# Performance work log

Hardware: AMD Instinct MI355X
Metric: run time of the kernel (lower is better)

Reference implementation:

```python
import jax, jax.numpy as jnp
import numpy as np

N_HEADS = 8
DIM_HEAD = 64


def _lin_params(key, fan_in, fan_out):
    k1, k2 = jax.random.split(key)
    w = jax.random.normal(k1, (fan_out, fan_in), jnp.float32) * 0.02
    b = jax.random.normal(k2, (fan_out,), jnp.float32) * 0.02
    return w, b


def setup_inputs() -> dict:
    key = jax.random.key(0)
    ks = jax.random.split(key, 16)
    n_nodes, n_edges = 30000, 480000
    input_nf, output_nf, hidden_nf = 128, 128, 256
    hd = N_HEADS * DIM_HEAD
    inp = {}
    inp['h'] = jax.random.normal(ks[0], (n_nodes, input_nf), jnp.float32)
    inp['x'] = jax.random.normal(ks[1], (n_nodes, 3), jnp.float32)
    inp['edge_index'] = jax.random.randint(ks[2], (2, n_edges), 0, n_nodes, jnp.int64)
    inp['mask'] = jnp.ones((n_edges,), jnp.bool_)
    inp['wq'], inp['bq'] = _lin_params(ks[3], input_nf, hd)
    inp['wk'], inp['bk'] = _lin_params(ks[4], input_nf, hd)
    inp['wv'], inp['bv'] = _lin_params(ks[5], input_nf, hd)
    inp['wo'], inp['bo'] = _lin_params(ks[6], hd, output_nf)
    inp['pw1'], inp['pb1'] = _lin_params(ks[7], 6, hidden_nf)
    inp['pw2'], inp['pb2'] = _lin_params(ks[8], hidden_nf, N_HEADS)
    inp['ew1'], inp['eb1'] = _lin_params(ks[9], 2 * input_nf + 7, hidden_nf)
    inp['ew2'], inp['eb2'] = _lin_params(ks[10], hidden_nf, hidden_nf)
    inp['eww'], inp['ewb'] = _lin_params(ks[11], hidden_nf, N_HEADS)
    inp['cw1'], inp['cb1'] = _lin_params(ks[12], 3, hidden_nf)
    inp['cw2'], inp['cb2'] = _lin_params(ks[13], hidden_nf, hidden_nf)
    inp['cw3'], inp['cb3'] = _lin_params(ks[14], hidden_nf, output_nf)
    return inp


def reference(h, x, edge_index, mask,
              wq, bq, wk, bk, wv, bv, wo, bo,
              pw1, pb1, pw2, pb2,
              ew1, eb1, ew2, eb2, eww, ewb,
              cw1, cb1, cw2, cb2, cw3, cb3):
    n_nodes = h.shape[0]
    row, col = edge_index[0], edge_index[1]
    # node projections -> [n, H, D]
    q = (h @ wq.T + bq).reshape(n_nodes, N_HEADS, DIM_HEAD)
    k = (h @ wk.T + bk).reshape(n_nodes, N_HEADS, DIM_HEAD)
    v = (h @ wv.T + bv).reshape(n_nodes, N_HEADS, DIM_HEAD)
    xr, xc = x[row], x[col]
    # pos encoding [E, H]
    abs_pos = jnp.concatenate([xr, xc], axis=-1)
    pos_enc = jax.nn.silu(abs_pos @ pw1.T + pb1) @ pw2.T + pb2
    # edge features -> per-head edge weights [E, H]
    rel_dist = jnp.sum((xr - xc) ** 2, axis=-1, keepdims=True)
    edge_attr = jnp.concatenate([h[row], h[col], rel_dist, xr, xc], axis=-1)
    edge_feat = jax.nn.silu(edge_attr @ ew1.T + eb1) @ ew2.T + eb2
    edge_w = edge_feat @ eww.T + ewb
    # attention scores [E, H]
    score = jnp.einsum('ehd,ehd->eh', q[row], k[col]) / (DIM_HEAD ** 0.5)
    score = score + pos_enc + edge_w
    score = jnp.where(mask[:, None], score, jnp.float32(-1e9))
    # scatter-softmax over edges grouped by destination (row)
    smax = jax.ops.segment_max(score, row, num_segments=n_nodes)
    escore = jnp.exp(score - smax[row])
    ssum = jax.ops.segment_sum(escore, row, num_segments=n_nodes)
    attn = escore / (ssum[row] + 1e-8)
    # weighted aggregation [n, H, D]
    agg = jax.ops.segment_sum(attn[:, :, None] * v[col], row, num_segments=n_nodes)
    out = agg.reshape(n_nodes, -1) @ wo.T + bo
    coord = jax.nn.silu(x @ cw1.T + cb1)
    coord = jax.nn.silu(coord @ cw2.T + cb2)
    coord = coord @ cw3.T + cb3
    return out + coord, jnp.zeros_like(x)
```

## Files before the change

### kernel.cpp

```cpp
#include <hip/hip_runtime.h>

typedef unsigned int uint;
typedef unsigned short ushort;
typedef unsigned char uchar;
typedef __attribute__((ext_vector_type(8))) short bf16x8;
typedef __attribute__((ext_vector_type(8))) ushort ushort8;
typedef __attribute__((ext_vector_type(4))) float f32x4;

__device__ __forceinline__ float silu_fast(float t) {
  return t * __builtin_amdgcn_rcpf(1.f + __expf(-t));
}
__device__ __forceinline__ float bf2f(ushort u) {
  union { uint i; float f; } v; v.i = ((uint)u) << 16; return v.f;
}
__device__ __forceinline__ ushort f2bf(float f) {
  union { float f; uint i; } v; v.f = f;
  uint r = (v.i + 0x7fffu + ((v.i >> 16) & 1u)) >> 16;
  return (ushort)r;
}
__device__ __forceinline__ uchar f2e4m3(float f) {
  uint u = __float_as_uint(f);
  uint s = (u >> 24) & 0x80u;
  uint m = u & 0x7fffffffu;
  if (m >= 0x43f00000u) return (uchar)(s | 0x7e);
  if (m >= 0x3c800000u) {
    uint r = m + 0x7ffffu + ((m >> 20) & 1u);
    uint e = (r >> 23) - 120u;
    if (e > 15u) return (uchar)(s | 0x7e);
    return (uchar)(s | (e << 3) | ((r >> 20) & 7u));
  }
  float az = __uint_as_float(m);
  uint k = (uint)__float2int_rn(az * 512.f);
  return (uchar)(s | k);
}
__device__ __forceinline__ float e4m3f(uint b) {
  uint u = ((b & 0x80u) << 24) | ((b & 0x7fu) << 20);
  return __uint_as_float(u) * 0x1p+120f;
}

__global__ __launch_bounds__(256) void mega_prep(
    const float* __restrict__ h, const float* __restrict__ x,
    const int* __restrict__ ei,
    const float* __restrict__ wq, const float* __restrict__ wk, const float* __restrict__ wv,
    const float* __restrict__ bq, const float* __restrict__ bk, const float* __restrict__ bv,
    const float* __restrict__ ew1, const float* __restrict__ eb1,
    const float* __restrict__ pw1, const float* __restrict__ pb1,
    const float* __restrict__ ew2, const float* __restrict__ eww,
    const float* __restrict__ eb2, const float* __restrict__ ewb,
    const float* __restrict__ pw2, const float* __restrict__ pb2,
    const float* __restrict__ wo, const float* __restrict__ cw3,
    const float* __restrict__ bo, const float* __restrict__ cb3,
    const float* __restrict__ cw1, const float* __restrict__ cb1,
    const float* __restrict__ cw2,
    ushort* __restrict__ h_bf, ushort* __restrict__ c1,
    ushort* __restrict__ wqkv, float* __restrict__ bqkv,
    short* __restrict__ W1T, float* __restrict__ b1big,
    short* __restrict__ W2T, float* __restrict__ biasC,
    ushort* __restrict__ wcomb, float* __restrict__ bcomb,
    ushort* __restrict__ cw2bf, int* __restrict__ cnt,
    int n, int E,
    int o1, int o2, int o3, int o4, int o5, int o6, int o7)
{
  int b = blockIdx.x, tid = threadIdx.x;
  if (b < o1) {
    int idx = b * 256 + tid;
    if (idx * 4 < n * 128) {
      float4 v = *(const float4*)(h + idx * 4);
      ushort4 o; o.x = f2bf(v.x); o.y = f2bf(v.y); o.z = f2bf(v.z); o.w = f2bf(v.w);
      *(ushort4*)(h_bf + idx * 4) = o;
    }
  } else if (b < o2) {
    int idx = (b - o1) * 256 + tid;
    if (idx < n * 256) {
      int node = idx >> 8, j = idx & 255;
      float t = fmaf(x[node * 3 + 2], cw1[j * 3 + 2],
                fmaf(x[node * 3 + 1], cw1[j * 3 + 1],
                fmaf(x[node * 3 + 0], cw1[j * 3 + 0], cb1[j])));
      c1[idx] = f2bf(silu_fast(t));
    }
  } else if (b < o3) {
    int idx = (b - o2) * 256 + tid;
    if (idx < 1536 * 128) {
      int j = idx >> 7, k = idx & 127;
      float v = (j < 512) ? wq[j * 128 + k]
              : (j < 1024) ? wk[(j - 512) * 128 + k]
              : wv[(j - 1024) * 128 + k];
      wqkv[idx] = f2bf(v);
      if (idx < 1536)
        bqkv[idx] = (idx < 512) ? bq[idx] : (idx < 1024) ? bk[idx - 512] : bv[idx - 1024];
    }
  } else if (b < o4) {
    int idx = (b - o3) * 256 + tid;
    if (idx < 512 * 288) {
      int nn = idx / 288, k = idx % 288;
      float v = 0.f;
      if (nn < 256) { if (k < 263) v = ew1[nn * 263 + k]; }
      else          { if (k >= 257 && k < 263) v = pw1[(nn - 256) * 6 + (k - 257)]; }
      W1T[idx] = (short)f2bf(v);
      if (idx < 512) b1big[idx] = (idx < 256) ? eb1[idx] : pb1[idx - 256];
    }
  } else if (b < o5) {
    int idx = (b - o4) * 256 + tid;
    if (idx < 16 * 512) {
      int hh = idx >> 9, k = idx & 511;
      float v = 0.f;
      if (hh < 8) {
        if (k < 256) {
          float s = 0.f;
          for (int j = 0; j < 256; ++j) s += eww[hh * 256 + j] * ew2[j * 256 + k];
          v = s;
        } else v = pw2[hh * 256 + (k - 256)];
      }
      W2T[idx] = (short)f2bf(v);
      if (idx < 16) {
        float bb = 0.f;
        if (idx < 8) {
          float s = 0.f;
          for (int j = 0; j < 256; ++j) s += eww[idx * 256 + j] * eb2[j];
          bb = s + ewb[idx] + pb2[idx];
        }
        biasC[idx] = bb;
      }
    }
  } else if (b < o6) {
    int idx = (b - o5) * 256 + tid;
    if (idx < 128 * 768) {
      int j = idx / 768, k = idx % 768;
      float v = (k < 512) ? wo[j * 512 + k] : cw3[j * 256 + (k - 512)];
      wcomb[idx] = f2bf(v);
      if (idx < 128) bcomb[idx] = bo[idx] + cb3[idx];
    }
  } else if (b < o7) {
    int idx = (b - o6) * 256 + tid;
    if (idx < 256 * 256) cw2bf[idx] = f2bf(cw2[idx]);
  } else {
    int e = (b - o7) * 256 + tid;
    if (e < E) atomicAdd(&cnt[ei[e]], 1);
  }
}

__global__ __launch_bounds__(256) void qkv_mfma2_kernel(
    const ushort* __restrict__ h_bf,
    const ushort* __restrict__ wqkv,
    const float* __restrict__ bqkv,
    ushort* __restrict__ q_t, uchar* __restrict__ k8, ushort* __restrict__ v_t,
    int n)
{
  int tid = threadIdx.x;
  int lane = tid & 63, w = tid >> 6;
  int l15 = lane & 15, l4 = lane >> 4;
  int m0 = blockIdx.x * 64;
  int mrow = m0 + w * 16 + l15;
  bool valid = mrow < n;
  int mr = valid ? mrow : (n - 1);

  bf16x8 hf[4];
#pragma unroll
  for (int ks = 0; ks < 4; ++ks)
    hf[ks] = *(const bf16x8*)(h_bf + (size_t)mr * 128 + ks * 32 + l4 * 8);

  for (int jb = 0; jb < 24; ++jb) {
    f32x4 acc[4];
#pragma unroll
    for (int nf = 0; nf < 4; ++nf) acc[nf] = (f32x4){0.f, 0.f, 0.f, 0.f};
#pragma unroll
    for (int nf = 0; nf < 4; ++nf)
#pragma unroll
      for (int ks = 0; ks < 4; ++ks) {
        bf16x8 wf = *(const bf16x8*)(wqkv + (size_t)(jb * 64 + nf * 16 + l15) * 128 + ks * 32 + l4 * 8);
        acc[nf] = __builtin_amdgcn_mfma_f32_16x16x32_bf16(wf, hf[ks], acc[nf], 0, 0, 0);
      }
    if (valid) {
#pragma unroll
      for (int nf = 0; nf < 4; ++nf) {
        int gc = jb * 64 + nf * 16 + l4 * 4;
        float4 bb = *(const float4*)(bqkv + gc);
        float v0 = acc[nf][0] + bb.x, v1 = acc[nf][1] + bb.y;
        float v2 = acc[nf][2] + bb.z, v3 = acc[nf][3] + bb.w;
        if (jb < 8) {
          ushort4 st; st.x = f2bf(v0); st.y = f2bf(v1); st.z = f2bf(v2); st.w = f2bf(v3);
          *(ushort4*)(q_t + (size_t)mrow * 512 + gc) = st;
        } else if (jb < 16) {
          uint pk = (uint)f2e4m3(v0) | ((uint)f2e4m3(v1) << 8)
                  | ((uint)f2e4m3(v2) << 16) | ((uint)f2e4m3(v3) << 24);
          *(uint*)(k8 + (size_t)mrow * 512 + (gc - 512)) = pk;
        } else {
          ushort4 st; st.x = f2bf(v0); st.y = f2bf(v1); st.z = f2bf(v2); st.w = f2bf(v3);
          *(ushort4*)(v_t + (size_t)mrow * 512 + (gc - 1024)) = st;
        }
      }
    }
  }
}

#define EB 64
#define GS 32
#define TS 72

__global__ __launch_bounds__(256, 4) void edge_mfma2_kernel(
    const ushort* __restrict__ h_bf, const float* __restrict__ x,
    const int* __restrict__ ei, int E,
    const short* __restrict__ W1T, const float* __restrict__ b1big,
    const short* __restrict__ W2T, const float* __restrict__ biasC,
    float* __restrict__ scores)
{
  __shared__ short geomL[EB * GS];
  __shared__ short T1[4 * EB * TS];
  float* slab = (float*)T1;

  int tid = threadIdx.x;
  int lane = tid & 63, w = tid >> 6;
  int l15 = lane & 15, l4 = lane >> 4;
  int eb0 = blockIdx.x * EB;

  if (tid < EB) {
    int eg = min(eb0 + tid, E - 1);
    int r = ei[eg], c = ei[E + eg];
    float xr0 = x[r*3], xr1 = x[r*3+1], xr2 = x[r*3+2];
    float xc0 = x[c*3], xc1 = x[c*3+1], xc2 = x[c*3+2];
    float d0 = xr0-xc0, d1 = xr1-xc1, d2 = xr2-xc2;
    bf16x8 g;
    g[0] = (short)f2bf(d0*d0 + d1*d1 + d2*d2);
    g[1] = (short)f2bf(xr0); g[2] = (short)f2bf(xr1); g[3] = (short)f2bf(xr2);
    g[4] = (short)f2bf(xc0); g[5] = (short)f2bf(xc1); g[6] = (short)f2bf(xc2);
    g[7] = 0;
    bf16x8 z = {0,0,0,0,0,0,0,0};
    *(bf16x8*)(geomL + tid * GS) = g;
    *(bf16x8*)(geomL + tid * GS + 8) = z;
    *(bf16x8*)(geomL + tid * GS + 16) = z;
    *(bf16x8*)(geomL + tid * GS + 24) = z;
  }
  __syncthreads();

  const char* hb = (const char*)h_bf;
  uint ro[4], co[4], ga[4];
#pragma unroll
  for (int ef = 0; ef < 4; ++ef) {
    int eg = min(eb0 + ef * 16 + l15, E - 1);
    int r = ei[eg], c = ei[E + eg];
    ro[ef] = (uint)r * 256 + l4 * 16;
    co[ef] = (uint)c * 256 + l4 * 16;
    ga[ef] = (uint)(ef * 16 + l15) * (GS * 2) + l4 * 16;
  }

  f32x4 sacc[4];
#pragma unroll
  for (int ef = 0; ef < 4; ++ef) sacc[ef] = (f32x4){0.f, 0.f, 0.f, 0.f};

  short* t1w = T1 + w * (EB * TS);

#pragma unroll
  for (int cch = 0; cch < 2; ++cch) {
    const int n0 = cch ? (256 + w * 64) : (w * 64);
    const int ks0 = cch ? 8 : 0;
    f32x4 acc[4][4];
#pragma unroll
    for (int mf = 0; mf < 4; ++mf)
#pragma unroll
      for (int ef = 0; ef < 4; ++ef) acc[mf][ef] = (f32x4){0.f, 0.f, 0.f, 0.f};

#pragma unroll
    for (int ks = ks0; ks < 9; ++ks) {
      bf16x8 aW[4], bE[4];
#pragma unroll
      for (int mf = 0; mf < 4; ++mf)
        aW[mf] = *(const bf16x8*)(W1T + (size_t)(n0 + mf * 16 + l15) * 288 + ks * 32 + l4 * 8);
#pragma unroll
      for (int ef = 0; ef < 4; ++ef) {
        if (ks < 4)      bE[ef] = *(const bf16x8*)(hb + ro[ef] + ks * 64);
        else if (ks < 8) bE[ef] = *(const bf16x8*)(hb + co[ef] + (ks - 4) * 64);
        else             bE[ef] = *(const bf16x8*)((const char*)geomL + ga[ef]);
      }
#pragma unroll
      for (int mf = 0; mf < 4; ++mf)
#pragma unroll
        for (int ef = 0; ef < 4; ++ef)
          acc[mf][ef] = __builtin_amdgcn_mfma_f32_16x16x32_bf16(aW[mf], bE[ef], acc[mf][ef], 0, 0, 0);
    }
#pragma unroll
    for (int mf = 0; mf < 4; ++mf) {
      int nl = mf * 16 + l4 * 4;
      float4 bias = *(const float4*)(b1big + n0 + nl);
#pragma unroll
      for (int ef = 0; ef < 4; ++ef) {
        int e = ef * 16 + l15;
        f32x4 v = acc[mf][ef];
        float s0 = silu_fast(v[0] + bias.x);
        float s1 = silu_fast(v[1] + bias.y);
        float s2 = silu_fast(v[2] + bias.z);
        float s3 = silu_fast(v[3] + bias.w);
        uint2 pk;
        asm("v_cvt_pk_bf16_f32 %0, %1, %2" : "=v"(pk.x) : "v"(s0), "v"(s1));
        asm("v_cvt_pk_bf16_f32 %0, %1, %2" : "=v"(pk.y) : "v"(s2), "v"(s3));
        *(uint2*)(t1w + e * TS + nl) = pk;
      }
    }
#pragma unroll
    for (int ks2 = 0; ks2 < 2; ++ks2) {
      bf16x8 bW2 = *(const bf16x8*)(W2T + (size_t)l15 * 512 + n0 + ks2 * 32 + l4 * 8);
#pragma unroll
      for (int ef = 0; ef < 4; ++ef) {
        bf16x8 aT = *(const bf16x8*)(t1w + (ef * 16 + l15) * TS + ks2 * 32 + l4 * 8);
        sacc[ef] = __builtin_amdgcn_mfma_f32_16x16x32_bf16(aT, bW2, sacc[ef], 0, 0, 0);
      }
    }
  }
  __syncthreads();
#pragma unroll
  for (int ef = 0; ef < 4; ++ef)
#pragma unroll
    for (int i = 0; i < 4; ++i)
      slab[(w * EB + ef * 16 + l4 * 4 + i) * 16 + l15] = sacc[ef][i];
  __syncthreads();
  for (int t = tid; t < EB * 8; t += 256) {
    int e = t >> 3, hh = t & 7;
    float s = biasC[hh]
            + slab[(0 * EB + e) * 16 + hh] + slab[(1 * EB + e) * 16 + hh]
            + slab[(2 * EB + e) * 16 + hh] + slab[(3 * EB + e) * 16 + hh];
    if (eb0 + e < E) scores[(size_t)(eb0 + e) * 8 + hh] = s;
  }
}

__global__ __launch_bounds__(1024) void scan_kernel(int* __restrict__ cnt,
                                                    int* __restrict__ offs, int n) {
  __shared__ int part[1024];
  int t = threadIdx.x;
  int chunk = (n + 1023) >> 10;
  int s = t * chunk, e = min(s + chunk, n);
  int sum = 0;
  for (int i = s; i < e; ++i) sum += cnt[i];
  part[t] = sum;
  __syncthreads();
  for (int off = 1; off < 1024; off <<= 1) {
    int v = (t >= off) ? part[t - off] : 0;
    __syncthreads();
    part[t] += v;
    __syncthreads();
  }
  int run = (t == 0) ? 0 : part[t - 1];
  for (int i = s; i < e; ++i) {
    int c = cnt[i];
    offs[i] = run;
    cnt[i] = run;
    run += c;
  }
  if (t == 1023) offs[n] = run;
}

__global__ __launch_bounds__(256) void fill_kernel(const int* __restrict__ ei,
                                                   int* __restrict__ cursor,
                                                   int2* __restrict__ pairs, int E) {
  int e = blockIdx.x * 256 + threadIdx.x;
  if (e < E) {
    int p = atomicAdd(&cursor[ei[e]], 1);
    pairs[p] = make_int2(e, ei[E + e]);
  }
}

__global__ __launch_bounds__(256) void attn_fused_kernel(
    const int* __restrict__ offs,
    const int2* __restrict__ pairs,
    const int* __restrict__ mask,
    const float* __restrict__ scores,
    const ushort* __restrict__ q_t,
    const uchar* __restrict__ k8,
    const ushort* __restrict__ v_t,
    ushort* __restrict__ agg, int n)
{
  int node = blockIdx.x * 4 + (threadIdx.x >> 6);
  if (node >= n) return;
  int lane = threadIdx.x & 63;
  int start = offs[node], end = offs[node + 1];

  bf16x8 qv = *(const bf16x8*)(q_t + (size_t)node * 512 + lane * 8);
  float qf[8];
#pragma unroll
  for (int j = 0; j < 8; ++j) qf[j] = bf2f((ushort)qv[j]);

  float m = -3.0e38f, ssum = 0.f;
  float acc[8];
#pragma unroll
  for (int j = 0; j < 8; ++j) acc[j] = 0.f;

  if (start < end) {
    int2 pr = pairs[start];
    uint2 kw = *(const uint2*)(k8 + (size_t)pr.y * 512 + lane * 8);
    bf16x8 vv = *(const bf16x8*)(v_t + (size_t)pr.y * 512 + lane * 8);
    float sml = scores[(size_t)pr.x * 8 + (lane >> 3)];
    int mk = mask[pr.x];

    for (int i = start; i < end; ++i) {
      uint2 kwc = kw; bf16x8 vvc = vv; float smlc = sml; int mkc = mk;
      int inx = (i + 1 < end) ? (i + 1) : i;
      pr = pairs[inx];
      kw = *(const uint2*)(k8 + (size_t)pr.y * 512 + lane * 8);
      vv = *(const bf16x8*)(v_t + (size_t)pr.y * 512 + lane * 8);
      sml = scores[(size_t)pr.x * 8 + (lane >> 3)];
      mk = mask[pr.x];

      float dot = 0.f;
#pragma unroll
      for (int j = 0; j < 4; ++j)
        dot = fmaf(qf[j], e4m3f((kwc.x >> (8 * j)) & 0xffu), dot);
#pragma unroll
      for (int j = 0; j < 4; ++j)
        dot = fmaf(qf[4 + j], e4m3f((kwc.y >> (8 * j)) & 0xffu), dot);
      dot += __shfl_xor(dot, 1);
      dot += __shfl_xor(dot, 2);
      dot += __shfl_xor(dot, 4);
      float s = mkc ? fmaf(dot, 0.125f, smlc) : -1e9f;
      float nm = fmaxf(m, s);
      float cs = __expf(m - nm);
      float e  = __expf(s - nm);
      ssum = fmaf(ssum, cs, e);
#pragma unroll
      for (int j = 0; j < 8; ++j)
        acc[j] = fmaf(acc[j], cs, e * bf2f((ushort)vvc[j]));
      m = nm;
    }
  }
  float inv = __builtin_amdgcn_rcpf(ssum + 1e-8f);
  ushort8 ov;
#pragma unroll
  for (int j = 0; j < 8; ++j) ov[j] = f2bf(acc[j] * inv);
  *(ushort8*)(agg + (size_t)node * 512 + lane * 8) = ov;
}

__global__ __launch_bounds__(256) void c2_mfma_kernel(const ushort* __restrict__ c1,
                                                      const ushort* __restrict__ cw2bf,
                                                      const float* __restrict__ cb2,
                                                      ushort* __restrict__ c2, int n) {
  __shared__ float oS[64 * 68];
  int tid = threadIdx.x;
  int lane = tid & 63, w = tid >> 6;
  int l15 = lane & 15, l4 = lane >> 4;
  int m0 = blockIdx.x * 64;
  int n0 = blockIdx.y * 64 + w * 16;

  f32x4 acc[4];
#pragma unroll
  for (int mf = 0; mf < 4; ++mf) acc[mf] = (f32x4){0.f, 0.f, 0.f, 0.f};
#pragma unroll
  for (int ks = 0; ks < 8; ++ks) {
    bf16x8 bW = *(const bf16x8*)(cw2bf + (size_t)(n0 + l15) * 256 + ks * 32 + l4 * 8);
#pragma unroll
    for (int mf = 0; mf < 4; ++mf) {
      int gr = m0 + mf * 16 + l15; if (gr >= n) gr = n - 1;
      bf16x8 aH = *(const bf16x8*)(c1 + (size_t)gr * 256 + ks * 32 + l4 * 8);
      acc[mf] = __builtin_amdgcn_mfma_f32_16x16x32_bf16(aH, bW, acc[mf], 0, 0, 0);
    }
  }
#pragma unroll
  for (int mf = 0; mf < 4; ++mf)
#pragma unroll
    for (int i = 0; i < 4; ++i)
      oS[(mf * 16 + l4 * 4 + i) * 68 + w * 16 + l15] = acc[mf][i];
  __syncthreads();
  {
    int row = tid >> 2, cs = (tid & 3) * 16;
    int gr = m0 + row;
    if (gr < n) {
      int gc = blockIdx.y * 64 + cs;
      ushort8 o0, o1;
#pragma unroll
      for (int j = 0; j < 8; ++j) o0[j] = f2bf(silu_fast(oS[row * 68 + cs + j] + cb2[gc + j]));
#pragma unroll
      for (int j = 0; j < 8; ++j) o1[j] = f2bf(silu_fast(oS[row * 68 + cs + 8 + j] + cb2[gc + 8 + j]));
      *(ushort8*)(c2 + (size_t)gr * 256 + gc) = o0;
      *(ushort8*)(c2 + (size_t)gr * 256 + gc + 8) = o1;
    }
  }
}

__global__ __launch_bounds__(256) void final_mfma_kernel(const ushort* __restrict__ agg,
                                                         const ushort* __restrict__ c2,
                                                         const ushort* __restrict__ wcomb,
                                                         const float* __restrict__ bcomb,
                                                         float* __restrict__ out, int n) {
  __shared__ float oS[64 * 68];
  int tid = threadIdx.x;
  int lane = tid & 63, w = tid >> 6;
  int l15 = lane & 15, l4 = lane >> 4;
  int m0 = blockIdx.x * 64;
  int jb = blockIdx.y;
  int n0 = jb * 64 + w * 16;

  f32x4 acc[4];
#pragma unroll
  for (int mf = 0; mf < 4; ++mf) acc[mf] = (f32x4){0.f, 0.f, 0.f, 0.f};
#pragma unroll
  for (int ks = 0; ks < 24; ++ks) {
    bf16x8 bW = *(const bf16x8*)(wcomb + (size_t)(n0 + l15) * 768 + ks * 32 + l4 * 8);
#pragma unroll
    for (int mf = 0; mf < 4; ++mf) {
      int gr = m0 + mf * 16 + l15; if (gr >= n) gr = n - 1;
      const ushort* ap = (ks < 16) ? (agg + (size_t)gr * 512 + ks * 32)
                                   : (c2 + (size_t)gr * 256 + (ks - 16) * 32);
      bf16x8 aH = *(const bf16x8*)(ap + l4 * 8);
      acc[mf] = __builtin_amdgcn_mfma_f32_16x16x32_bf16(aH, bW, acc[mf], 0, 0, 0);
    }
  }
#pragma unroll
  for (int mf = 0; mf < 4; ++mf)
#pragma unroll
    for (int i = 0; i < 4; ++i)
      oS[(mf * 16 + l4 * 4 + i) * 68 + w * 16 + l15] = acc[mf][i];
  __syncthreads();
  {
    int row = tid >> 2, cs = (tid & 3) * 16;
    int gr = m0 + row;
    if (gr < n) {
      int gc = jb * 64 + cs;
#pragma unroll
      for (int g = 0; g < 4; ++g) {
        float4 o;
        o.x = oS[row * 68 + cs + g * 4 + 0] + bcomb[gc + g * 4 + 0];
        o.y = oS[row * 68 + cs + g * 4 + 1] + bcomb[gc + g * 4 + 1];
        o.z = oS[row * 68 + cs + g * 4 + 2] + bcomb[gc + g * 4 + 2];
        o.w = oS[row * 68 + cs + g * 4 + 3] + bcomb[gc + g * 4 + 3];
        *(float4*)(out + (size_t)gr * 128 + gc + g * 4) = o;
      }
    }
  }
}

extern "C" void kernel_launch(void* const* d_in, const int* in_sizes, int n_in,
                              void* d_out, int out_size, void* d_ws, size_t ws_size,
                              hipStream_t stream) {
  const float* h   = (const float*)d_in[0];
  const float* x   = (const float*)d_in[1];
  const int*   ei  = (const int*)d_in[2];
  const int*   mask= (const int*)d_in[3];
  const float* wq  = (const float*)d_in[4];
  const float* bq  = (const float*)d_in[5];
  const float* wk  = (const float*)d_in[6];
  const float* bk  = (const float*)d_in[7];
  const float* wv  = (const float*)d_in[8];
  const float* bv  = (const float*)d_in[9];
  const float* wo  = (const float*)d_in[10];
  const float* bo  = (const float*)d_in[11];
  const float* pw1 = (const float*)d_in[12];
  const float* pb1 = (const float*)d_in[13];
  const float* pw2 = (const float*)d_in[14];
  const float* pb2 = (const float*)d_in[15];
  const float* ew1 = (const float*)d_in[16];
  const float* eb1 = (const float*)d_in[17];
  const float* ew2 = (const float*)d_in[18];
  const float* eb2 = (const float*)d_in[19];
  const float* eww = (const float*)d_in[20];
  const float* ewb = (const float*)d_in[21];
  const float* cw1 = (const float*)d_in[22];
  const float* cb1 = (const float*)d_in[23];
  const float* cw2 = (const float*)d_in[24];
  const float* cb2 = (const float*)d_in[25];
  const float* cw3 = (const float*)d_in[26];
  const float* cb3 = (const float*)d_in[27];

  int n = in_sizes[0] / 128;
  int E = in_sizes[3];

  char* wptr = (char*)d_ws;
  auto alloc = [&](size_t bytes) {
    char* p = wptr;
    wptr += (bytes + 255) & ~(size_t)255;
    return p;
  };
  ushort* q_t   = (ushort*)alloc((size_t)n * 512 * 2);
  uchar*  k8    = (uchar*)alloc((size_t)n * 512);
  ushort* v_t   = (ushort*)alloc((size_t)n * 512 * 2);
  ushort* h_bf  = (ushort*)alloc((size_t)n * 128 * 2);
  float* scores = (float*)alloc((size_t)E * 8 * 4);
  ushort* agg   = (ushort*)alloc((size_t)n * 512 * 2);
  ushort* c1    = (ushort*)alloc((size_t)n * 256 * 2);
  ushort* c2    = (ushort*)alloc((size_t)n * 256 * 2);
  ushort* wqkv  = (ushort*)alloc((size_t)1536 * 128 * 2);
  float* bqkv   = (float*)alloc((size_t)1536 * 4);
  short* W1T    = (short*)alloc((size_t)512 * 288 * 2);
  float* b1big  = (float*)alloc((size_t)512 * 4);
  short* W2T    = (short*)alloc((size_t)16 * 512 * 2);
  float* biasC  = (float*)alloc((size_t)16 * 4);
  ushort* wcomb = (ushort*)alloc((size_t)128 * 768 * 2);
  float* bcomb  = (float*)alloc((size_t)128 * 4);
  ushort* cw2bf = (ushort*)alloc((size_t)256 * 256 * 2);
  int* offs     = (int*)alloc((size_t)(n + 1) * 4);
  int* cursor   = (int*)alloc((size_t)n * 4);
  int2* pairs   = (int2*)alloc((size_t)E * 8);

  hipMemsetAsync(cursor, 0, (size_t)n * 4, stream);

  int b_h2  = (n * 128 / 4 + 255) / 256;
  int b_c1  = (n * 256 + 255) / 256;
  int b_wq  = (1536 * 128 + 255) / 256;
  int b_w1  = (512 * 288 + 255) / 256;
  int b_w2  = (16 * 512 + 255) / 256;
  int b_wc  = (128 * 768 + 255) / 256;
  int b_cw  = (256 * 256 + 255) / 256;
  int b_cnt = (E + 255) / 256;
  int o1 = b_h2, o2 = o1 + b_c1, o3 = o2 + b_wq, o4 = o3 + b_w1;
  int o5 = o4 + b_w2, o6 = o5 + b_wc, o7 = o6 + b_cw;
  int total_blocks = o7 + b_cnt;

  mega_prep<<<dim3(total_blocks), 256, 0, stream>>>(
      h, x, ei, wq, wk, wv, bq, bk, bv, ew1, eb1, pw1, pb1, ew2, eww, eb2, ewb,
      pw2, pb2, wo, cw3, bo, cb3, cw1, cb1, cw2,
      h_bf, c1, wqkv, bqkv, W1T, b1big, W2T, biasC, wcomb, bcomb, cw2bf, cursor,
      n, E, o1, o2, o3, o4, o5, o6, o7);

  scan_kernel<<<dim3(1), 1024, 0, stream>>>(cursor, offs, n);
  fill_kernel<<<dim3((E + 255) / 256), 256, 0, stream>>>(ei, cursor, pairs, E);

  qkv_mfma2_kernel<<<dim3((n + 63) / 64), 256, 0, stream>>>(h_bf, wqkv, bqkv, q_t, k8, v_t, n);

  edge_mfma2_kernel<<<dim3((E + EB - 1) / EB), 256, 0, stream>>>(
      h_bf, x, ei, E, W1T, b1big, W2T, biasC, scores);

  attn_fused_kernel<<<dim3((n + 3) / 4), 256, 0, stream>>>(
      offs, pairs, mask, scores, q_t, k8, v_t, agg, n);

  c2_mfma_kernel<<<dim3((n + 63) / 64, 4), 256, 0, stream>>>(c1, cw2bf, cb2, c2, n);

  hipMemsetAsync((float*)d_out + (size_t)n * 128, 0, (size_t)n * 3 * 4, stream);
  final_mfma_kernel<<<dim3((n + 63) / 64, 2), 256, 0, stream>>>(agg, c2, wcomb, bcomb,
                                                                (float*)d_out, n);
}
```

Before: 701.0 us.

## Factor edge MLP first layer into per-node projections gathered per edge

The first edge-MLP layer applied to [h[row], h[col]] is split algebraically into two node-level projections (P1 = h·W_row, P2 = h·W_col). These are computed in the node projection GEMM alongside Q/K/V, so each edge only gathers two 256-wide bf16 rows instead of doing a K=256 GEMM. The edge kernel now walks edges in CSR (sorted) order, folds the mask into the pairs array, and writes scores contiguously so attention reads them sequentially. The separate h-to-bf16 conversion pass goes away, and agg reuses the q_t buffer. In exchange it adds bf16 rounding of the partial sums and extra node-level storage.

```diff
diff --git a/kernel.cpp b/kernel.cpp
--- a/kernel.cpp
+++ b/kernel.cpp
@@ -13,10 +13,19 @@
 __device__ __forceinline__ float bf2f(ushort u) {
   union { uint i; float f; } v; v.i = ((uint)u) << 16; return v.f;
 }
+__device__ __forceinline__ float bf2f_lo(uint u) {
+  union { uint i; float f; } v; v.i = u << 16; return v.f;
+}
+__device__ __forceinline__ float bf2f_hi(uint u) {
+  union { uint i; float f; } v; v.i = u & 0xffff0000u; return v.f;
+}
 __device__ __forceinline__ ushort f2bf(float f) {
   union { float f; uint i; } v; v.f = f;
   uint r = (v.i + 0x7fffu + ((v.i >> 16) & 1u)) >> 16;
   return (ushort)r;
+}
+__device__ __forceinline__ uint cvtpk_bf(float a, float b) {
+  uint r; asm("v_cvt_pk_bf16_f32 %0, %1, %2" : "=v"(r) : "v"(a), "v"(b)); return r;
 }
 __device__ __forceinline__ uchar f2e4m3(float f) {
   uint u = __float_as_uint(f);
@@ -39,8 +48,7 @@
 }
 
 __global__ __launch_bounds__(256) void mega_prep(
-    const float* __restrict__ h, const float* __restrict__ x,
-    const int* __restrict__ ei,
+    const float* __restrict__ x, const int* __restrict__ ei,
     const float* __restrict__ wq, const float* __restrict__ wk, const float* __restrict__ wv,
     const float* __restrict__ bq, const float* __restrict__ bk, const float* __restrict__ bv,
     const float* __restrict__ ew1, const float* __restrict__ eb1,
@@ -52,25 +60,18 @@
     const float* __restrict__ bo, const float* __restrict__ cb3,
     const float* __restrict__ cw1, const float* __restrict__ cb1,
     const float* __restrict__ cw2,
-    ushort* __restrict__ h_bf, ushort* __restrict__ c1,
-    ushort* __restrict__ wqkv, float* __restrict__ bqkv,
-    short* __restrict__ W1T, float* __restrict__ b1big,
+    ushort* __restrict__ c1,
+    ushort* __restrict__ wnode, float* __restrict__ bqkv,
+    short* __restrict__ W1g,
     short* __restrict__ W2T, float* __restrict__ biasC,
     ushort* __restrict__ wcomb, float* __restrict__ bcomb,
     ushort* __restrict__ cw2bf, int* __restrict__ cnt,
     int n, int E,
-    int o1, int o2, int o3, int o4, int o5, int o6, int o7)
+    int o1, int o2, int o3, int o4, int o5, int o6)
 {
   int b = blockIdx.x, tid = threadIdx.x;
   if (b < o1) {
     int idx = b * 256 + tid;
-    if (idx * 4 < n * 128) {
-      float4 v = *(const float4*)(h + idx * 4);
-      ushort4 o; o.x = f2bf(v.x); o.y = f2bf(v.y); o.z = f2bf(v.z); o.w = f2bf(v.w);
-      *(ushort4*)(h_bf + idx * 4) = o;
-    }
-  } else if (b < o2) {
-    int idx = (b - o1) * 256 + tid;
     if (idx < n * 256) {
       int node = idx >> 8, j = idx & 255;
       float t = fmaf(x[node * 3 + 2], cw1[j * 3 + 2],
@@ -78,29 +79,37 @@
                 fmaf(x[node * 3 + 0], cw1[j * 3 + 0], cb1[j])));
       c1[idx] = f2bf(silu_fast(t));
     }
+  } else if (b < o2) {
+    int idx = (b - o1) * 256 + tid;
+    if (idx < 2048 * 128) {
+      int j = idx >> 7, k = idx & 127;
+      float v;
+      if (j < 512)       v = wq[j * 128 + k];
+      else if (j < 1024) v = wk[(j - 512) * 128 + k];
+      else if (j < 1536) v = wv[(j - 1024) * 128 + k];
+      else if (j < 1792) v = ew1[(j - 1536) * 263 + k];
+      else               v = ew1[(j - 1792) * 263 + 128 + k];
+      wnode[idx] = f2bf(v);
+      if (idx < 1536)
+        bqkv[idx] = (idx < 512) ? bq[idx] : (idx < 1024) ? bk[idx - 512] : bv[idx - 1024];
+    }
   } else if (b < o3) {
     int idx = (b - o2) * 256 + tid;
-    if (idx < 1536 * 128) {
-      int j = idx >> 7, k = idx & 127;
-      float v = (j < 512) ? wq[j * 128 + k]
-              : (j < 1024) ? wk[(j - 512) * 128 + k]
-              : wv[(j - 1024) * 128 + k];
-      wqkv[idx] = f2bf(v);
-      if (idx < 1536)
-        bqkv[idx] = (idx < 512) ? bq[idx] : (idx < 1024) ? bk[idx - 512] : bv[idx - 1024];
+    if (idx < 512 * 32) {
+      int nn = idx >> 5, k = idx & 31;
+      float v = 0.f;
+      if (nn < 256) {
+        if (k == 0)      v = eb1[nn];
+        else if (k < 8)  v = ew1[nn * 263 + 256 + (k - 1)];
+      } else {
+        int p = nn - 256;
+        if (k == 0)           v = pb1[p];
+        else if (k >= 2 && k < 8) v = pw1[p * 6 + (k - 2)];
+      }
+      W1g[idx] = (short)f2bf(v);
     }
   } else if (b < o4) {
     int idx = (b - o3) * 256 + tid;
-    if (idx < 512 * 288) {
-      int nn = idx / 288, k = idx % 288;
-      float v = 0.f;
-      if (nn < 256) { if (k < 263) v = ew1[nn * 263 + k]; }
-      else          { if (k >= 257 && k < 263) v = pw1[(nn - 256) * 6 + (k - 257)]; }
-      W1T[idx] = (short)f2bf(v);
-      if (idx < 512) b1big[idx] = (idx < 256) ? eb1[idx] : pb1[idx - 256];
-    }
-  } else if (b < o5) {
-    int idx = (b - o4) * 256 + tid;
     if (idx < 16 * 512) {
       int hh = idx >> 9, k = idx & 511;
       float v = 0.f;
@@ -122,44 +131,54 @@
         biasC[idx] = bb;
       }
     }
-  } else if (b < o6) {
-    int idx = (b - o5) * 256 + tid;
+  } else if (b < o5) {
+    int idx = (b - o4) * 256 + tid;
     if (idx < 128 * 768) {
       int j = idx / 768, k = idx % 768;
       float v = (k < 512) ? wo[j * 512 + k] : cw3[j * 256 + (k - 512)];
       wcomb[idx] = f2bf(v);
       if (idx < 128) bcomb[idx] = bo[idx] + cb3[idx];
     }
-  } else if (b < o7) {
-    int idx = (b - o6) * 256 + tid;
+  } else if (b < o6) {
+    int idx = (b - o5) * 256 + tid;
     if (idx < 256 * 256) cw2bf[idx] = f2bf(cw2[idx]);
   } else {
-    int e = (b - o7) * 256 + tid;
+    int e = (b - o6) * 256 + tid;
     if (e < E) atomicAdd(&cnt[ei[e]], 1);
   }
 }
 
-__global__ __launch_bounds__(256) void qkv_mfma2_kernel(
-    const ushort* __restrict__ h_bf,
-    const ushort* __restrict__ wqkv,
+__global__ __launch_bounds__(256) void nodeproj_kernel(
+    const float* __restrict__ h,
+    const ushort* __restrict__ wnode,
     const float* __restrict__ bqkv,
     ushort* __restrict__ q_t, uchar* __restrict__ k8, ushort* __restrict__ v_t,
+    ushort* __restrict__ P1t, ushort* __restrict__ P2t,
     int n)
 {
   int tid = threadIdx.x;
   int lane = tid & 63, w = tid >> 6;
   int l15 = lane & 15, l4 = lane >> 4;
   int m0 = blockIdx.x * 64;
+  int jb0 = blockIdx.y * 8;
   int mrow = m0 + w * 16 + l15;
   bool valid = mrow < n;
   int mr = valid ? mrow : (n - 1);
 
   bf16x8 hf[4];
 #pragma unroll
-  for (int ks = 0; ks < 4; ++ks)
-    hf[ks] = *(const bf16x8*)(h_bf + (size_t)mr * 128 + ks * 32 + l4 * 8);
-
-  for (int jb = 0; jb < 24; ++jb) {
+  for (int ks = 0; ks < 4; ++ks) {
+    const float* hp = h + (size_t)mr * 128 + ks * 32 + l4 * 8;
+    float4 a0 = *(const float4*)hp;
+    float4 a1 = *(const float4*)(hp + 4);
+    uint4 pk;
+    pk.x = cvtpk_bf(a0.x, a0.y); pk.y = cvtpk_bf(a0.z, a0.w);
+    pk.z = cvtpk_bf(a1.x, a1.y); pk.w = cvtpk_bf(a1.z, a1.w);
+    union { uint4 u; bf16x8 b; } cv; cv.u = pk;
+    hf[ks] = cv.b;
+  }
+
+  for (int jb = jb0; jb < jb0 + 8; ++jb) {
     f32x4 acc[4];
 #pragma unroll
     for (int nf = 0; nf < 4; ++nf) acc[nf] = (f32x4){0.f, 0.f, 0.f, 0.f};
@@ -167,157 +186,38 @@
     for (int nf = 0; nf < 4; ++nf)
 #pragma unroll
       for (int ks = 0; ks < 4; ++ks) {
-        bf16x8 wf = *(const bf16x8*)(wqkv + (size_t)(jb * 64 + nf * 16 + l15) * 128 + ks * 32 + l4 * 8);
+        bf16x8 wf = *(const bf16x8*)(wnode + (size_t)(jb * 64 + nf * 16 + l15) * 128 + ks * 32 + l4 * 8);
         acc[nf] = __builtin_amdgcn_mfma_f32_16x16x32_bf16(wf, hf[ks], acc[nf], 0, 0, 0);
       }
     if (valid) {
 #pragma unroll
       for (int nf = 0; nf < 4; ++nf) {
         int gc = jb * 64 + nf * 16 + l4 * 4;
-        float4 bb = *(const float4*)(bqkv + gc);
-        float v0 = acc[nf][0] + bb.x, v1 = acc[nf][1] + bb.y;
-        float v2 = acc[nf][2] + bb.z, v3 = acc[nf][3] + bb.w;
-        if (jb < 8) {
-          ushort4 st; st.x = f2bf(v0); st.y = f2bf(v1); st.z = f2bf(v2); st.w = f2bf(v3);
-          *(ushort4*)(q_t + (size_t)mrow * 512 + gc) = st;
-        } else if (jb < 16) {
-          uint pk = (uint)f2e4m3(v0) | ((uint)f2e4m3(v1) << 8)
-                  | ((uint)f2e4m3(v2) << 16) | ((uint)f2e4m3(v3) << 24);
-          *(uint*)(k8 + (size_t)mrow * 512 + (gc - 512)) = pk;
+        if (jb < 24) {
+          float4 bb = *(const float4*)(bqkv + gc);
+          float v0 = acc[nf][0] + bb.x, v1 = acc[nf][1] + bb.y;
+          float v2 = acc[nf][2] + bb.z, v3 = acc[nf][3] + bb.w;
+          if (jb < 8) {
+            ushort4 st; st.x = f2bf(v0); st.y = f2bf(v1); st.z = f2bf(v2); st.w = f2bf(v3);
+            *(ushort4*)(q_t + (size_t)mrow * 512 + gc) = st;
+          } else if (jb < 16) {
+            uint pk = (uint)f2e4m3(v0) | ((uint)f2e4m3(v1) << 8)
+                    | ((uint)f2e4m3(v2) << 16) | ((uint)f2e4m3(v3) << 24);
+            *(uint*)(k8 + (size_t)mrow * 512 + (gc - 512)) = pk;
+          } else {
+            ushort4 st; st.x = f2bf(v0); st.y = f2bf(v1); st.z = f2bf(v2); st.w = f2bf(v3);
+            *(ushort4*)(v_t + (size_t)mrow * 512 + (gc - 1024)) = st;
+          }
         } else {
-          ushort4 st; st.x = f2bf(v0); st.y = f2bf(v1); st.z = f2bf(v2); st.w = f2bf(v3);
-          *(ushort4*)(v_t + (size_t)mrow * 512 + (gc - 1024)) = st;
+          int pc = (jb & 3) * 64 + nf * 16 + l4 * 4;
+          ushort4 st;
+          st.x = f2bf(acc[nf][0]); st.y = f2bf(acc[nf][1]);
+          st.z = f2bf(acc[nf][2]); st.w = f2bf(acc[nf][3]);
+          if (jb < 28) *(ushort4*)(P1t + (size_t)mrow * 256 + pc) = st;
+          else         *(ushort4*)(P2t + (size_t)mrow * 256 + pc) = st;
         }
       }
     }
-  }
-}
-
-#define EB 64
-#define GS 32
-#define TS 72
-
-__global__ __launch_bounds__(256, 4) void edge_mfma2_kernel(
-    const ushort* __restrict__ h_bf, const float* __restrict__ x,
-    const int* __restrict__ ei, int E,
-    const short* __restrict__ W1T, const float* __restrict__ b1big,
-    const short* __restrict__ W2T, const float* __restrict__ biasC,
-    float* __restrict__ scores)
-{
-  __shared__ short geomL[EB * GS];
-  __shared__ short T1[4 * EB * TS];
-  float* slab = (float*)T1;
-
-  int tid = threadIdx.x;
-  int lane = tid & 63, w = tid >> 6;
-  int l15 = lane & 15, l4 = lane >> 4;
-  int eb0 = blockIdx.x * EB;
-
-  if (tid < EB) {
-    int eg = min(eb0 + tid, E - 1);
-    int r = ei[eg], c = ei[E + eg];
-    float xr0 = x[r*3], xr1 = x[r*3+1], xr2 = x[r*3+2];
-    float xc0 = x[c*3], xc1 = x[c*3+1], xc2 = x[c*3+2];
-    float d0 = xr0-xc0, d1 = xr1-xc1, d2 = xr2-xc2;
-    bf16x8 g;
-    g[0] = (short)f2bf(d0*d0 + d1*d1 + d2*d2);
-    g[1] = (short)f2bf(xr0); g[2] = (short)f2bf(xr1); g[3] = (short)f2bf(xr2);
-    g[4] = (short)f2bf(xc0); g[5] = (short)f2bf(xc1); g[6] = (short)f2bf(xc2);
-    g[7] = 0;
-    bf16x8 z = {0,0,0,0,0,0,0,0};
-    *(bf16x8*)(geomL + tid * GS) = g;
-    *(bf16x8*)(geomL + tid * GS + 8) = z;
-    *(bf16x8*)(geomL + tid * GS + 16) = z;
-    *(bf16x8*)(geomL + tid * GS + 24) = z;
-  }
-  __syncthreads();
-
-  const char* hb = (const char*)h_bf;
-  uint ro[4], co[4], ga[4];
-#pragma unroll
-  for (int ef = 0; ef < 4; ++ef) {
-    int eg = min(eb0 + ef * 16 + l15, E - 1);
-    int r = ei[eg], c = ei[E + eg];
-    ro[ef] = (uint)r * 256 + l4 * 16;
-    co[ef] = (uint)c * 256 + l4 * 16;
-    ga[ef] = (uint)(ef * 16 + l15) * (GS * 2) + l4 * 16;
-  }
-
-  f32x4 sacc[4];
-#pragma unroll
-  for (int ef = 0; ef < 4; ++ef) sacc[ef] = (f32x4){0.f, 0.f, 0.f, 0.f};
-
-  short* t1w = T1 + w * (EB * TS);
-
-#pragma unroll
-  for (int cch = 0; cch < 2; ++cch) {
-    const int n0 = cch ? (256 + w * 64) : (w * 64);
-    const int ks0 = cch ? 8 : 0;
-    f32x4 acc[4][4];
-#pragma unroll
-    for (int mf = 0; mf < 4; ++mf)
-#pragma unroll
-      for (int ef = 0; ef < 4; ++ef) acc[mf][ef] = (f32x4){0.f, 0.f, 0.f, 0.f};
-
-#pragma unroll
-    for (int ks = ks0; ks < 9; ++ks) {
-      bf16x8 aW[4], bE[4];
-#pragma unroll
-      for (int mf = 0; mf < 4; ++mf)
-        aW[mf] = *(const bf16x8*)(W1T + (size_t)(n0 + mf * 16 + l15) * 288 + ks * 32 + l4 * 8);
-#pragma unroll
-      for (int ef = 0; ef < 4; ++ef) {
-        if (ks < 4)      bE[ef] = *(const bf16x8*)(hb + ro[ef] + ks * 64);
-        else if (ks < 8) bE[ef] = *(const bf16x8*)(hb + co[ef] + (ks - 4) * 64);
-        else             bE[ef] = *(const bf16x8*)((const char*)geomL + ga[ef]);
-      }
-#pragma unroll
-      for (int mf = 0; mf < 4; ++mf)
-#pragma unroll
-        for (int ef = 0; ef < 4; ++ef)
-          acc[mf][ef] = __builtin_amdgcn_mfma_f32_16x16x32_bf16(aW[mf], bE[ef], acc[mf][ef], 0, 0, 0);
-    }
-#pragma unroll
-    for (int mf = 0; mf < 4; ++mf) {
-      int nl = mf * 16 + l4 * 4;
-      float4 bias = *(const float4*)(b1big + n0 + nl);
-#pragma unroll
-      for (int ef = 0; ef < 4; ++ef) {
-        int e = ef * 16 + l15;
-        f32x4 v = acc[mf][ef];
-        float s0 = silu_fast(v[0] + bias.x);
-        float s1 = silu_fast(v[1] + bias.y);
-        float s2 = silu_fast(v[2] + bias.z);
-        float s3 = silu_fast(v[3] + bias.w);
-        uint2 pk;
-        asm("v_cvt_pk_bf16_f32 %0, %1, %2" : "=v"(pk.x) : "v"(s0), "v"(s1));
-        asm("v_cvt_pk_bf16_f32 %0, %1, %2" : "=v"(pk.y) : "v"(s2), "v"(s3));
-        *(uint2*)(t1w + e * TS + nl) = pk;
-      }
-    }
-#pragma unroll
-    for (int ks2 = 0; ks2 < 2; ++ks2) {
-      bf16x8 bW2 = *(const bf16x8*)(W2T + (size_t)l15 * 512 + n0 + ks2 * 32 + l4 * 8);
-#pragma unroll
-      for (int ef = 0; ef < 4; ++ef) {
-        bf16x8 aT = *(const bf16x8*)(t1w + (ef * 16 + l15) * TS + ks2 * 32 + l4 * 8);
-        sacc[ef] = __builtin_amdgcn_mfma_f32_16x16x32_bf16(aT, bW2, sacc[ef], 0, 0, 0);
-      }
-    }
-  }
-  __syncthreads();
-#pragma unroll
-  for (int ef = 0; ef < 4; ++ef)
-#pragma unroll
-    for (int i = 0; i < 4; ++i)
-      slab[(w * EB + ef * 16 + l4 * 4 + i) * 16 + l15] = sacc[ef][i];
-  __syncthreads();
-  for (int t = tid; t < EB * 8; t += 256) {
-    int e = t >> 3, hh = t & 7;
-    float s = biasC[hh]
-            + slab[(0 * EB + e) * 16 + hh] + slab[(1 * EB + e) * 16 + hh]
-            + slab[(2 * EB + e) * 16 + hh] + slab[(3 * EB + e) * 16 + hh];
-    if (eb0 + e < E) scores[(size_t)(eb0 + e) * 8 + hh] = s;
   }
 }
 
@@ -348,19 +248,157 @@
 }
 
 __global__ __launch_bounds__(256) void fill_kernel(const int* __restrict__ ei,
+                                                   const int* __restrict__ mask,
                                                    int* __restrict__ cursor,
                                                    int2* __restrict__ pairs, int E) {
   int e = blockIdx.x * 256 + threadIdx.x;
   if (e < E) {
-    int p = atomicAdd(&cursor[ei[e]], 1);
-    pairs[p] = make_int2(e, ei[E + e]);
+    int r = ei[e];
+    int p = atomicAdd(&cursor[r], 1);
+    int rm = r | (mask[e] ? 0 : (int)0x80000000u);
+    pairs[p] = make_int2(ei[E + e], rm);
+  }
+}
+
+#define EB 64
+#define GS 40
+#define TS 72
+
+__global__ __launch_bounds__(256) void edge_mfma3_kernel(
+    const float* __restrict__ x,
+    const int2* __restrict__ pairs, int E,
+    const short* __restrict__ W1g,
+    const short* __restrict__ W2T, const float* __restrict__ biasC,
+    const ushort* __restrict__ P1t, const ushort* __restrict__ P2t,
+    float* __restrict__ scores)
+{
+  __shared__ short geomL[EB * GS];
+  __shared__ int2 rcL[EB];
+  __shared__ short T1[4 * EB * TS];
+  float* slab = (float*)T1;
+
+  int tid = threadIdx.x;
+  int lane = tid & 63, w = tid >> 6;
+  int l15 = lane & 15, l4 = lane >> 4;
+  int eb0 = blockIdx.x * EB;
+
+  if (tid < EB) {
+    int i = min(eb0 + tid, E - 1);
+    int2 pr = pairs[i];
+    rcL[tid] = pr;
+    int c = pr.x, r = pr.y & 0x7fffffff;
+    float xr0 = x[r*3], xr1 = x[r*3+1], xr2 = x[r*3+2];
+    float xc0 = x[c*3], xc1 = x[c*3+1], xc2 = x[c*3+2];
+    float d0 = xr0-xc0, d1 = xr1-xc1, d2 = xr2-xc2;
+    bf16x8 g;
+    g[0] = (short)0x3F80;
+    g[1] = (short)f2bf(d0*d0 + d1*d1 + d2*d2);
+    g[2] = (short)f2bf(xr0); g[3] = (short)f2bf(xr1); g[4] = (short)f2bf(xr2);
+    g[5] = (short)f2bf(xc0); g[6] = (short)f2bf(xc1); g[7] = (short)f2bf(xc2);
+    bf16x8 z = {0,0,0,0,0,0,0,0};
+    *(bf16x8*)(geomL + tid * GS) = g;
+    *(bf16x8*)(geomL + tid * GS + 8) = z;
+    *(bf16x8*)(geomL + tid * GS + 16) = z;
+    *(bf16x8*)(geomL + tid * GS + 24) = z;
+    *(bf16x8*)(geomL + tid * GS + 32) = z;
+  }
+  __syncthreads();
+
+  int rr[4], cc[4];
+  bf16x8 bE[4];
+#pragma unroll
+  for (int ef = 0; ef < 4; ++ef) {
+    int2 pr = rcL[ef * 16 + l15];
+    cc[ef] = pr.x; rr[ef] = pr.y & 0x7fffffff;
+    bE[ef] = *(const bf16x8*)(geomL + (ef * 16 + l15) * GS + l4 * 8);
+  }
+
+  f32x4 sacc[4];
+#pragma unroll
+  for (int ef = 0; ef < 4; ++ef) sacc[ef] = (f32x4){0.f, 0.f, 0.f, 0.f};
+
+  short* t1w = T1 + w * (EB * TS);
+
+#pragma unroll
+  for (int cch = 0; cch < 2; ++cch) {
+    const int n0 = cch ? (256 + w * 64) : (w * 64);
+    f32x4 acc[4][4];
+#pragma unroll
+    for (int mf = 0; mf < 4; ++mf) {
+      bf16x8 aW = *(const bf16x8*)(W1g + (size_t)(n0 + mf * 16 + l15) * 32 + l4 * 8);
+#pragma unroll
+      for (int ef = 0; ef < 4; ++ef)
+        acc[mf][ef] = __builtin_amdgcn_mfma_f32_16x16x32_bf16(
+            aW, bE[ef], (f32x4){0.f, 0.f, 0.f, 0.f}, 0, 0, 0);
+    }
+    if (cch == 0) {
+#pragma unroll
+      for (int mf = 0; mf < 4; ++mf) {
+        int colb = n0 + mf * 16 + l4 * 4;
+        uint2 g1[4], g2[4];
+#pragma unroll
+        for (int ef = 0; ef < 4; ++ef) {
+          g1[ef] = *(const uint2*)(P1t + (size_t)rr[ef] * 256 + colb);
+          g2[ef] = *(const uint2*)(P2t + (size_t)cc[ef] * 256 + colb);
+        }
+#pragma unroll
+        for (int ef = 0; ef < 4; ++ef) {
+          f32x4 a = acc[mf][ef];
+          a[0] += bf2f_lo(g1[ef].x) + bf2f_lo(g2[ef].x);
+          a[1] += bf2f_hi(g1[ef].x) + bf2f_hi(g2[ef].x);
+          a[2] += bf2f_lo(g1[ef].y) + bf2f_lo(g2[ef].y);
+          a[3] += bf2f_hi(g1[ef].y) + bf2f_hi(g2[ef].y);
+          acc[mf][ef] = a;
+        }
+      }
+    }
+#pragma unroll
+    for (int mf = 0; mf < 4; ++mf) {
+      int nl = mf * 16 + l4 * 4;
+#pragma unroll
+      for (int ef = 0; ef < 4; ++ef) {
+        int e = ef * 16 + l15;
+        f32x4 v = acc[mf][ef];
+        float s0 = silu_fast(v[0]);
+        float s1 = silu_fast(v[1]);
+        float s2 = silu_fast(v[2]);
+        float s3 = silu_fast(v[3]);
+        uint2 pk;
+        pk.x = cvtpk_bf(s0, s1);
+        pk.y = cvtpk_bf(s2, s3);
+        *(uint2*)(t1w + e * TS + nl) = pk;
+      }
+    }
+#pragma unroll
+    for (int ks2 = 0; ks2 < 2; ++ks2) {
+      bf16x8 bW2 = *(const bf16x8*)(W2T + (size_t)l15 * 512 + n0 + ks2 * 32 + l4 * 8);
+#pragma unroll
+      for (int ef = 0; ef < 4; ++ef) {
+        bf16x8 aT = *(const bf16x8*)(t1w + (ef * 16 + l15) * TS + ks2 * 32 + l4 * 8);
+        sacc[ef] = __builtin_amdgcn_mfma_f32_16x16x32_bf16(aT, bW2, sacc[ef], 0, 0, 0);
+      }
+    }
+  }
+  __syncthreads();
+#pragma unroll
+  for (int ef = 0; ef < 4; ++ef)
+#pragma unroll
+    for (int i = 0; i < 4; ++i)
+      slab[(w * EB + ef * 16 + l4 * 4 + i) * 16 + l15] = sacc[ef][i];
+  __syncthreads();
+  for (int t = tid; t < EB * 8; t += 256) {
+    int e = t >> 3, hh = t & 7;
+    float s = biasC[hh]
+            + slab[(0 * EB + e) * 16 + hh] + slab[(1 * EB + e) * 16 + hh]
+            + slab[(2 * EB + e) * 16 + hh] + slab[(3 * EB + e) * 16 + hh];
+    if (rcL[e].y < 0) s = -1e9f;
+    if (eb0 + e < E) scores[(size_t)(eb0 + e) * 8 + hh] = s;
   }
 }
 
 __global__ __launch_bounds__(256) void attn_fused_kernel(
     const int* __restrict__ offs,
     const int2* __restrict__ pairs,
-    const int* __restrict__ mask,
     const float* __restrict__ scores,
     const ushort* __restrict__ q_t,
     const uchar* __restrict__ k8,
@@ -383,20 +421,18 @@
   for (int j = 0; j < 8; ++j) acc[j] = 0.f;
 
   if (start < end) {
-    int2 pr = pairs[start];
-    uint2 kw = *(const uint2*)(k8 + (size_t)pr.y * 512 + lane * 8);
-    bf16x8 vv = *(const bf16x8*)(v_t + (size_t)pr.y * 512 + lane * 8);
-    float sml = scores[(size_t)pr.x * 8 + (lane >> 3)];
-    int mk = mask[pr.x];
+    int col = pairs[start].x;
+    uint2 kw = *(const uint2*)(k8 + (size_t)col * 512 + lane * 8);
+    bf16x8 vv = *(const bf16x8*)(v_t + (size_t)col * 512 + lane * 8);
+    float sml = scores[(size_t)start * 8 + (lane >> 3)];
 
     for (int i = start; i < end; ++i) {
-      uint2 kwc = kw; bf16x8 vvc = vv; float smlc = sml; int mkc = mk;
+      uint2 kwc = kw; bf16x8 vvc = vv; float smlc = sml;
       int inx = (i + 1 < end) ? (i + 1) : i;
-      pr = pairs[inx];
-      kw = *(const uint2*)(k8 + (size_t)pr.y * 512 + lane * 8);
-      vv = *(const bf16x8*)(v_t + (size_t)pr.y * 512 + lane * 8);
-      sml = scores[(size_t)pr.x * 8 + (lane >> 3)];
-      mk = mask[pr.x];
+      col = pairs[inx].x;
+      kw = *(const uint2*)(k8 + (size_t)col * 512 + lane * 8);
+      vv = *(const bf16x8*)(v_t + (size_t)col * 512 + lane * 8);
+      sml = scores[(size_t)inx * 8 + (lane >> 3)];
 
       float dot = 0.f;
 #pragma unroll
@@ -408,7 +444,7 @@
       dot += __shfl_xor(dot, 1);
       dot += __shfl_xor(dot, 2);
       dot += __shfl_xor(dot, 4);
-      float s = mkc ? fmaf(dot, 0.125f, smlc) : -1e9f;
+      float s = (smlc < -5e8f) ? -1e9f : fmaf(dot, 0.125f, smlc);
       float nm = fmaxf(m, s);
       float cs = __expf(m - nm);
       float e  = __expf(s - nm);
@@ -568,15 +604,14 @@
   ushort* q_t   = (ushort*)alloc((size_t)n * 512 * 2);
   uchar*  k8    = (uchar*)alloc((size_t)n * 512);
   ushort* v_t   = (ushort*)alloc((size_t)n * 512 * 2);
-  ushort* h_bf  = (ushort*)alloc((size_t)n * 128 * 2);
+  ushort* P1t   = (ushort*)alloc((size_t)n * 256 * 2);
+  ushort* P2t   = (ushort*)alloc((size_t)n * 256 * 2);
   float* scores = (float*)alloc((size_t)E * 8 * 4);
-  ushort* agg   = (ushort*)alloc((size_t)n * 512 * 2);
   ushort* c1    = (ushort*)alloc((size_t)n * 256 * 2);
   ushort* c2    = (ushort*)alloc((size_t)n * 256 * 2);
-  ushort* wqkv  = (ushort*)alloc((size_t)1536 * 128 * 2);
+  ushort* wnode = (ushort*)alloc((size_t)2048 * 128 * 2);
   float* bqkv   = (float*)alloc((size_t)1536 * 4);
-  short* W1T    = (short*)alloc((size_t)512 * 288 * 2);
-  float* b1big  = (float*)alloc((size_t)512 * 4);
+  short* W1g    = (short*)alloc((size_t)512 * 32 * 2);
   short* W2T    = (short*)alloc((size_t)16 * 512 * 2);
   float* biasC  = (float*)alloc((size_t)16 * 4);
   ushort* wcomb = (ushort*)alloc((size_t)128 * 768 * 2);
@@ -585,37 +620,38 @@
   int* offs     = (int*)alloc((size_t)(n + 1) * 4);
   int* cursor   = (int*)alloc((size_t)n * 4);
   int2* pairs   = (int2*)alloc((size_t)E * 8);
+  ushort* agg   = q_t;
 
   hipMemsetAsync(cursor, 0, (size_t)n * 4, stream);
 
-  int b_h2  = (n * 128 / 4 + 255) / 256;
   int b_c1  = (n * 256 + 255) / 256;
-  int b_wq  = (1536 * 128 + 255) / 256;
-  int b_w1  = (512 * 288 + 255) / 256;
+  int b_wn  = (2048 * 128) / 256;
+  int b_w1  = (512 * 32 + 255) / 256;
   int b_w2  = (16 * 512 + 255) / 256;
   int b_wc  = (128 * 768 + 255) / 256;
   int b_cw  = (256 * 256 + 255) / 256;
   int b_cnt = (E + 255) / 256;
-  int o1 = b_h2, o2 = o1 + b_c1, o3 = o2 + b_wq, o4 = o3 + b_w1;
-  int o5 = o4 + b_w2, o6 = o5 + b_wc, o7 = o6 + b_cw;
-  int total_blocks = o7 + b_cnt;
+  int o1 = b_c1, o2 = o1 + b_wn, o3 = o2 + b_w1, o4 = o3 + b_w2;
+  int o5 = o4 + b_wc, o6 = o5 + b_cw;
+  int total_blocks = o6 + b_cnt;
 
   mega_prep<<<dim3(total_blocks), 256, 0, stream>>>(
-      h, x, ei, wq, wk, wv, bq, bk, bv, ew1, eb1, pw1, pb1, ew2, eww, eb2, ewb,
+      x, ei, wq, wk, wv, bq, bk, bv, ew1, eb1, pw1, pb1, ew2, eww, eb2, ewb,
       pw2, pb2, wo, cw3, bo, cb3, cw1, cb1, cw2,
-      h_bf, c1, wqkv, bqkv, W1T, b1big, W2T, biasC, wcomb, bcomb, cw2bf, cursor,
-      n, E, o1, o2, o3, o4, o5, o6, o7);
+      c1, wnode, bqkv, W1g, W2T, biasC, wcomb, bcomb, cw2bf, cursor,
+      n, E, o1, o2, o3, o4, o5, o6);
 
   scan_kernel<<<dim3(1), 1024, 0, stream>>>(cursor, offs, n);
-  fill_kernel<<<dim3((E + 255) / 256), 256, 0, stream>>>(ei, cursor, pairs, E);
-
-  qkv_mfma2_kernel<<<dim3((n + 63) / 64), 256, 0, stream>>>(h_bf, wqkv, bqkv, q_t, k8, v_t, n);
-
-  edge_mfma2_kernel<<<dim3((E + EB - 1) / EB), 256, 0, stream>>>(
-      h_bf, x, ei, E, W1T, b1big, W2T, biasC, scores);
+  fill_kernel<<<dim3((E + 255) / 256), 256, 0, stream>>>(ei, mask, cursor, pairs, E);
+
+  nodeproj_kernel<<<dim3((n + 63) / 64, 4), 256, 0, stream>>>(
+      h, wnode, bqkv, q_t, k8, v_t, P1t, P2t, n);
+
+  edge_mfma3_kernel<<<dim3((E + EB - 1) / EB), 256, 0, stream>>>(
+      x, pairs, E, W1g, W2T, biasC, P1t, P2t, scores);
 
   attn_fused_kernel<<<dim3((n + 3) / 4), 256, 0, stream>>>(
-      offs, pairs, mask, scores, q_t, k8, v_t, agg, n);
+      offs, pairs, scores, q_t, k8, v_t, agg, n);
 
   c2_mfma_kernel<<<dim3((n + 63) / 64, 4), 256, 0, stream>>>(c1, cw2bf, cb2, c2, n);
 
```

Result: faster. 620.8 us (-11.4%).
